# Performance work log

Measured on AMD Instinct MI355X. Metric: run time of the kernel, lower is better.

Reference implementation:

```python
import jax, jax.numpy as jnp
import numpy as np

SH_C0 = 0.28209479177387814
EPS2D = 0.3      # gsplat low-pass filter added to 2D covariance diagonal
NEAR = 0.01
ALPHA_MIN = 1.0 / 255.0
ALPHA_MAX = 0.999


def setup_inputs() -> dict:
    key = jax.random.key(0)
    ks = jax.random.split(key, 5)
    N = 2048
    means = 0.1 * jax.random.normal(ks[0], (N, 3), jnp.float32)
    quats = jax.random.normal(ks[1], (N, 4), jnp.float32)
    scales = -2.3 + 0.3 * jax.random.normal(ks[2], (N, 3), jnp.float32)
    opacities = -1.0 + 0.5 * jax.random.normal(ks[3], (N,), jnp.float32)
    sh_coeffs = jax.random.normal(ks[4], (N, 1, 3), jnp.float32)
    viewmats = jnp.eye(4, dtype=jnp.float32).at[2, 3].set(2.0)[None]  # [1,4,4] world->cam
    Ks = jnp.array([[[150.0, 0.0, 64.0], [0.0, 150.0, 64.0], [0.0, 0.0, 1.0]]], jnp.float32)
    return dict(means=means, quats=quats, scales=scales, opacities=opacities,
                sh_coeffs=sh_coeffs, viewmats=viewmats, Ks=Ks, width=128, height=128)


def _splat_render(means, quats, scales, opacities, sh_coeffs, viewmats, Ks, width, height):
    # --- parameter activations (GaussianSplat.activated_parameters) ---
    quats = quats / jnp.linalg.norm(quats, axis=-1, keepdims=True)
    scales = jnp.minimum(jnp.exp(scales), 10.0)
    opac = jax.nn.sigmoid(opacities)                                  # [N]
    colors = jnp.maximum(sh_coeffs[:, 0, :] * SH_C0 + 0.5, 0.0)       # [N,3] sh_degree=0

    # --- 3D covariance from quaternion (w,x,y,z) and scale ---
    w, x, y, z = quats[:, 0], quats[:, 1], quats[:, 2], quats[:, 3]
    R = jnp.stack([
        1 - 2 * (y * y + z * z), 2 * (x * y - w * z), 2 * (x * z + w * y),
        2 * (x * y + w * z), 1 - 2 * (x * x + z * z), 2 * (y * z - w * x),
        2 * (x * z - w * y), 2 * (y * z + w * x), 1 - 2 * (x * x + y * y)],
        axis=-1).reshape(-1, 3, 3)                                    # [N,3,3]
    M = R * scales[:, None, :]                                        # R @ diag(s)
    cov3d = jnp.einsum('nij,nkj->nik', M, M)                          # [N,3,3]

    # --- project to camera frame ---
    Rcw = viewmats[:, :3, :3]                                         # [C,3,3]
    tcw = viewmats[:, :3, 3]                                          # [C,3]
    p_cam = jnp.einsum('cij,nj->cni', Rcw, means) + tcw[:, None, :]   # [C,N,3]
    Vc = jnp.einsum('cij,njk,clk->cnil', Rcw, cov3d, Rcw)             # [C,N,3,3]

    xc, yc, zc = p_cam[..., 0], p_cam[..., 1], p_cam[..., 2]
    valid = zc > NEAR
    zs = jnp.where(valid, zc, 1.0)
    rz = 1.0 / zs
    fx = Ks[:, 0, 0][:, None]; fy = Ks[:, 1, 1][:, None]
    cx = Ks[:, 0, 2][:, None]; cy = Ks[:, 1, 2][:, None]
    u = fx * xc * rz + cx                                             # [C,N]
    v = fy * yc * rz + cy

    # --- EWA 2D covariance: J Vc J^T + eps2d*I, J = d(proj)/d(p_cam) ---
    J00 = fx * rz; J02 = -fx * xc * rz * rz
    J11 = fy * rz; J12 = -fy * yc * rz * rz
    V00, V01, V02 = Vc[..., 0, 0], Vc[..., 0, 1], Vc[..., 0, 2]
    V11, V12, V22 = Vc[..., 1, 1], Vc[..., 1, 2], Vc[..., 2, 2]
    a = J00 * J00 * V00 + 2 * J00 * J02 * V02 + J02 * J02 * V22 + EPS2D
    b = J00 * (J11 * V01 + J12 * V02) + J02 * (J11 * V12 + J12 * V22)
    c = J11 * J11 * V11 + 2 * J11 * J12 * V12 + J12 * J12 * V22 + EPS2D
    det = a * c - b * b
    valid = valid & (det > 0)
    det_s = jnp.where(valid, det, 1.0)
    conA = c / det_s; conB = -b / det_s; conC = a / det_s             # conic (inverse cov)

    # --- per-pixel gaussian evaluation (pixel centers at +0.5) ---
    px = jnp.arange(width, dtype=jnp.float32) + 0.5                   # [W]
    py = jnp.arange(height, dtype=jnp.float32) + 0.5                  # [H]
    dx = px[None, None, :] - u[..., None]                             # [C,N,W]
    dy = py[None, None, :] - v[..., None]                             # [C,N,H]
    sigma = (0.5 * (conA[..., None, None] * (dx * dx)[:, :, None, :]
                    + conC[..., None, None] * (dy * dy)[..., None])
             + conB[..., None, None] * dy[..., None] * dx[:, :, None, :])  # [C,N,H,W]
    alpha = opac[None, :, None, None] * jnp.exp(-sigma)
    alpha = jnp.minimum(alpha, ALPHA_MAX)
    alpha = jnp.where(valid[..., None, None] & (alpha >= ALPHA_MIN), alpha, 0.0)

    # --- front-to-back alpha compositing in depth order ---
    order = jnp.argsort(jnp.where(valid, zc, jnp.inf), axis=1)        # [C,N]
    alpha_s = jnp.take_along_axis(alpha, order[:, :, None, None], axis=1)
    colors_s = jnp.take_along_axis(jnp.broadcast_to(colors[None], (alpha.shape[0],) + colors.shape),
                                   order[:, :, None], axis=1)         # [C,N,3]
    logT = jnp.cumsum(jnp.log1p(-alpha_s), axis=1)
    logT_excl = jnp.pad(logT, ((0, 0), (1, 0), (0, 0), (0, 0)))[:, :-1]
    weights = alpha_s * jnp.exp(logT_excl)                            # [C,N,H,W]
    img = jnp.einsum('cnhw,cnk->chwk', weights, colors_s)             # [C,H,W,3]
    return img


def reference(means, quats, scales, opacities, sh_coeffs, viewmats, Ks, width, height):
    return _splat_render(means, quats, scales, opacities, sh_coeffs, viewmats, Ks, width, height)
```

## Files before the change

### kernel.cpp

```cpp
#include <hip/hip_runtime.h>
#include <math.h>

#define SH_C0     0.28209479177387814f
#define EPS2D     0.3f
#define NEARZ     0.01f
#define ALPHA_MIN (1.0f/255.0f)
#define ALPHA_MAX 0.999f
#define LOG2E     1.4426950408889634f

#define SEGS   32
#define HSEG   16

__global__ __launch_bounds__(256) void prep_rank_kernel(
        const float* __restrict__ means,
        const float* __restrict__ quats,
        const float* __restrict__ scales,
        const float* __restrict__ opacities,
        const float* __restrict__ sh,
        const float* __restrict__ vm,
        const float* __restrict__ K,
        float* __restrict__ sorted,
        int N) {
    int wave = blockIdx.x * 4 + (threadIdx.x >> 6);
    int lane = threadIdx.x & 63;
    if (wave >= N) return;
    int i = wave;

    float r00=vm[0], r01=vm[1], r02=vm[2],  t0=vm[3];
    float r10=vm[4], r11=vm[5], r12=vm[6],  t1=vm[7];
    float r20=vm[8], r21=vm[9], r22=vm[10], t2=vm[11];

    float mx = means[3*i+0], my = means[3*i+1], mz = means[3*i+2];
    float zci = r20*mx + r21*my + r22*mz + t2;
    float keyi = (zci > NEARZ) ? zci : INFINITY;
    int cnt = 0;
    for (int j = lane; j < N; j += 64) {
        float ax = means[3*j+0], ay = means[3*j+1], az = means[3*j+2];
        float zcj = r20*ax + r21*ay + r22*az + t2;
        float keyj = (zcj > NEARZ) ? zcj : INFINITY;
        cnt += (keyj < keyi) || (keyj == keyi && j < i);
    }
    #pragma unroll
    for (int off = 32; off > 0; off >>= 1)
        cnt += __shfl_xor(cnt, off, 64);

    float qw = quats[4*i+0], qx = quats[4*i+1], qy = quats[4*i+2], qz = quats[4*i+3];
    float rqn = rsqrtf(qw*qw + qx*qx + qy*qy + qz*qz);
    qw *= rqn; qx *= rqn; qy *= rqn; qz *= rqn;

    float R00 = 1.f - 2.f*(qy*qy + qz*qz);
    float R01 = 2.f*(qx*qy - qw*qz);
    float R02 = 2.f*(qx*qz + qw*qy);
    float R10 = 2.f*(qx*qy + qw*qz);
    float R11 = 1.f - 2.f*(qx*qx + qz*qz);
    float R12 = 2.f*(qy*qz - qw*qx);
    float R20 = 2.f*(qx*qz - qw*qy);
    float R21 = 2.f*(qy*qz + qw*qx);
    float R22 = 1.f - 2.f*(qx*qx + qy*qy);

    float s0 = fminf(expf(scales[3*i+0]), 10.f);
    float s1 = fminf(expf(scales[3*i+1]), 10.f);
    float s2 = fminf(expf(scales[3*i+2]), 10.f);

    float M00=R00*s0, M01=R01*s1, M02=R02*s2;
    float M10=R10*s0, M11=R11*s1, M12=R12*s2;
    float M20=R20*s0, M21=R21*s1, M22=R22*s2;

    float c00 = M00*M00 + M01*M01 + M02*M02;
    float c01 = M00*M10 + M01*M11 + M02*M12;
    float c02 = M00*M20 + M01*M21 + M02*M22;
    float c11 = M10*M10 + M11*M11 + M12*M12;
    float c12 = M10*M20 + M11*M21 + M12*M22;
    float c22 = M20*M20 + M21*M21 + M22*M22;

    float xc = r00*mx + r01*my + r02*mz + t0;
    float yc = r10*mx + r11*my + r12*mz + t1;
    float zc = zci;

    float T00 = r00*c00 + r01*c01 + r02*c02;
    float T01 = r00*c01 + r01*c11 + r02*c12;
    float T02 = r00*c02 + r01*c12 + r02*c22;
    float T10 = r10*c00 + r11*c01 + r12*c02;
    float T11 = r10*c01 + r11*c11 + r12*c12;
    float T12 = r10*c02 + r11*c12 + r12*c22;
    float T20 = r20*c00 + r21*c01 + r22*c02;
    float T21 = r20*c01 + r21*c11 + r22*c12;
    float T22 = r20*c02 + r21*c12 + r22*c22;
    float V00 = T00*r00 + T01*r01 + T02*r02;
    float V01 = T00*r10 + T01*r11 + T02*r12;
    float V02 = T00*r20 + T01*r21 + T02*r22;
    float V11 = T10*r10 + T11*r11 + T12*r12;
    float V12 = T10*r20 + T11*r21 + T12*r22;
    float V22 = T20*r20 + T21*r21 + T22*r22;

    float fx = K[0], cx = K[2], fy = K[4], cy = K[5];

    bool valid = zc > NEARZ;
    float zs = valid ? zc : 1.0f;
    float rz = 1.0f / zs;
    float u = fx*xc*rz + cx;
    float v = fy*yc*rz + cy;
    float J00 = fx*rz;
    float J02 = -fx*xc*rz*rz;
    float J11 = fy*rz;
    float J12 = -fy*yc*rz*rz;

    float a = J00*J00*V00 + 2.f*J00*J02*V02 + J02*J02*V22 + EPS2D;
    float b = J00*(J11*V01 + J12*V02) + J02*(J11*V12 + J12*V22);
    float c = J11*J11*V11 + 2.f*J11*J12*V12 + J12*J12*V22 + EPS2D;
    float det = a*c - b*b;
    valid = valid && (det > 0.f);
    float det_s = valid ? det : 1.0f;
    float conA =  c / det_s;
    float conB = -b / det_s;
    float conC =  a / det_s;

    float op  = 1.0f / (1.0f + expf(-opacities[i]));
    float cr = fmaxf(sh[3*i+0]*SH_C0 + 0.5f, 0.f);
    float cg = fmaxf(sh[3*i+1]*SH_C0 + 0.5f, 0.f);
    float cb = fmaxf(sh[3*i+2]*SH_C0 + 0.5f, 0.f);

    float e0, e1, e2, e3, e4, e5;
    if (valid) {
        e0 = u; e1 = v;
        e2 = 0.5f*conA*LOG2E; e3 = conB*LOG2E; e4 = 0.5f*conC*LOG2E;
        e5 = log2f(op);
    } else {
        e0=0; e1=0; e2=0; e3=0; e4=0; e5=-1.0e4f;
    }

    if (lane < 16) {
        float val;
        switch (lane) {
            case 0: val = e0; break;
            case 1: val = e1; break;
            case 2: val = e2; break;
            case 3: val = e3; break;
            case 4: val = e4; break;
            case 5: val = e5; break;
            case 6: val = cr; break;
            case 7: val = cg; break;
            case 8: val = cb; break;
            default: val = 0.f; break;
        }
        sorted[16*(size_t)cnt + lane] = val;
    }
}

__global__ __launch_bounds__(1024) void render_main_kernel(
        const float* __restrict__ sorted,
        float4* __restrict__ parts,
        int N, int P) {
    __shared__ float4 part[HSEG][64];
    int tid  = threadIdx.x;
    int lane = tid & 63;
    int w    = __builtin_amdgcn_readfirstlane(tid >> 6);
    int h    = blockIdx.x & 1;
    int pg   = blockIdx.x >> 1;
    int p    = pg * 64 + lane;

    int y = p >> 7;
    int x = p & 127;
    float px = (float)x + 0.5f;
    float py = (float)y + 0.5f;

    int chunk = (N + SEGS - 1) / SEGS;
    int s  = h * HSEG + w;
    int g0 = s * chunk;
    int g1 = min(g0 + chunk, N);

    float accr = 0.f, accg = 0.f, accb = 0.f, T = 1.f;
    #pragma unroll 4
    for (int g = g0; g < g1; ++g) {
        const float* d = sorted + 16*(size_t)g;
        float u  = d[0], v  = d[1];
        float A2 = d[2], B  = d[3], C2 = d[4], lop = d[5];
        float cr = d[6], cg = d[7], cb = d[8];
        float dx = px - u, dy = py - v;
        float t2  = fmaf(A2, dx, B*dy);
        float arg = fmaf(-C2, dy*dy, lop);
        arg = fmaf(-dx, t2, arg);
        float al = exp2f(arg);
        al = fminf(al, ALPHA_MAX);
        al = (al >= ALPHA_MIN) ? al : 0.f;
        float wgt = T * al;
        accr = fmaf(wgt, cr, accr);
        accg = fmaf(wgt, cg, accg);
        accb = fmaf(wgt, cb, accb);
        T = fmaf(-al, T, T);
    }
    part[w][lane] = make_float4(accr, accg, accb, T);
    __syncthreads();

    if (tid < 64) {
        float R = 0.f, G = 0.f, Bc = 0.f, Tr = 1.f;
        #pragma unroll
        for (int ss = 0; ss < HSEG; ++ss) {
            float4 q = part[ss][tid];
            R  = fmaf(Tr, q.x, R);
            G  = fmaf(Tr, q.y, G);
            Bc = fmaf(Tr, q.z, Bc);
            Tr *= q.w;
        }
        parts[(size_t)h * P + p] = make_float4(R, G, Bc, Tr);
    }
}

__global__ __launch_bounds__(256) void combine_kernel(
        const float4* __restrict__ parts,
        float* __restrict__ out, int P) {
    int p = blockIdx.x * 256 + threadIdx.x;
    if (p >= P) return;
    float4 a = parts[p];
    float4 b = parts[(size_t)P + p];
    out[3*(size_t)p+0] = fmaf(a.w, b.x, a.x);
    out[3*(size_t)p+1] = fmaf(a.w, b.y, a.y);
    out[3*(size_t)p+2] = fmaf(a.w, b.z, a.z);
}

extern "C" void kernel_launch(void* const* d_in, const int* in_sizes, int n_in,
                              void* d_out, int out_size, void* d_ws, size_t ws_size,
                              hipStream_t stream) {
    const float* means     = (const float*)d_in[0];
    const float* quats     = (const float*)d_in[1];
    const float* scales    = (const float*)d_in[2];
    const float* opacities = (const float*)d_in[3];
    const float* sh        = (const float*)d_in[4];
    const float* vm        = (const float*)d_in[5];
    const float* K         = (const float*)d_in[6];

    int N = in_sizes[0] / 3;
    int P = out_size / 3;

    float*  sorted = (float*)d_ws;
    float4* parts  = (float4*)((float*)d_ws + (size_t)N * 16);

    prep_rank_kernel<<<(N + 3) / 4, 256, 0, stream>>>(
        means, quats, scales, opacities, sh, vm, K, sorted, N);
    render_main_kernel<<<((P + 63) / 64) * 2, 1024, 0, stream>>>(
        sorted, parts, N, P);
    combine_kernel<<<(P + 255) / 256, 256, 0, stream>>>(
        parts, (float*)d_out, P);
}
```

Measured before the change: 102.8 us.

## Split render into four 512-thread layers with packed 48-byte float4 records

The render kernel moves from two 1024-thread halves to four 512-thread layers of 8 waves each, and the combine kernel now composites four partial layers. Gaussian records shrink from 16 to 12 floats and are read as three float4 loads. Opacity is stored linearly and multiplied after a raw hardware exp2, so the per-gaussian add of log-opacity becomes a multiply. The aim is better occupancy and fewer load instructions, at the cost of more combine traffic and slightly different alpha rounding.

Measured after the change: 95.46 us. -7.2%, faster.

```diff
diff --git a/kernel.cpp b/kernel.cpp
--- a/kernel.cpp
+++ b/kernel.cpp
@@ -9,7 +9,8 @@
 #define LOG2E     1.4426950408889634f
 
 #define SEGS   32
-#define HSEG   16
+#define LSEG   8
+#define NLAYER 4
 
 __global__ __launch_bounds__(256) void prep_rank_kernel(
         const float* __restrict__ means,
@@ -124,69 +125,69 @@
     if (valid) {
         e0 = u; e1 = v;
         e2 = 0.5f*conA*LOG2E; e3 = conB*LOG2E; e4 = 0.5f*conC*LOG2E;
-        e5 = log2f(op);
+        e5 = op;
     } else {
-        e0=0; e1=0; e2=0; e3=0; e4=0; e5=-1.0e4f;
-    }
-
-    if (lane < 16) {
+        e0=0; e1=0; e2=0; e3=0; e4=0; e5=0;
+    }
+
+    if (lane < 12) {
         float val;
         switch (lane) {
-            case 0: val = e0; break;
-            case 1: val = e1; break;
-            case 2: val = e2; break;
-            case 3: val = e3; break;
-            case 4: val = e4; break;
-            case 5: val = e5; break;
-            case 6: val = cr; break;
-            case 7: val = cg; break;
-            case 8: val = cb; break;
+            case 0:  val = e0; break;
+            case 1:  val = e1; break;
+            case 2:  val = e2; break;
+            case 3:  val = e3; break;
+            case 4:  val = e4; break;
+            case 5:  val = e5; break;
+            case 6:  val = cr; break;
+            case 7:  val = cg; break;
+            case 8:  val = cb; break;
             default: val = 0.f; break;
         }
-        sorted[16*(size_t)cnt + lane] = val;
-    }
-}
-
-__global__ __launch_bounds__(1024) void render_main_kernel(
+        sorted[12*(size_t)cnt + lane] = val;
+    }
+}
+
+__global__ __launch_bounds__(512, 8) void render_main_kernel(
         const float* __restrict__ sorted,
         float4* __restrict__ parts,
         int N, int P) {
-    __shared__ float4 part[HSEG][64];
+    __shared__ float4 part[LSEG][64];
     int tid  = threadIdx.x;
     int lane = tid & 63;
     int w    = __builtin_amdgcn_readfirstlane(tid >> 6);
-    int h    = blockIdx.x & 1;
-    int pg   = blockIdx.x >> 1;
+    int L    = blockIdx.x & (NLAYER - 1);
+    int pg   = blockIdx.x >> 2;
     int p    = pg * 64 + lane;
 
-    int y = p >> 7;
-    int x = p & 127;
-    float px = (float)x + 0.5f;
-    float py = (float)y + 0.5f;
+    float px = (float)(p & 127) + 0.5f;
+    float py = (float)(p >> 7) + 0.5f;
 
     int chunk = (N + SEGS - 1) / SEGS;
-    int s  = h * HSEG + w;
+    int s  = L * LSEG + w;
     int g0 = s * chunk;
     int g1 = min(g0 + chunk, N);
 
+    const float4* rec = (const float4*)sorted + 3*(size_t)g0;
+
     float accr = 0.f, accg = 0.f, accb = 0.f, T = 1.f;
-    #pragma unroll 4
+    #pragma unroll 2
     for (int g = g0; g < g1; ++g) {
-        const float* d = sorted + 16*(size_t)g;
-        float u  = d[0], v  = d[1];
-        float A2 = d[2], B  = d[3], C2 = d[4], lop = d[5];
-        float cr = d[6], cg = d[7], cb = d[8];
-        float dx = px - u, dy = py - v;
-        float t2  = fmaf(A2, dx, B*dy);
-        float arg = fmaf(-C2, dy*dy, lop);
-        arg = fmaf(-dx, t2, arg);
-        float al = exp2f(arg);
+        float4 r0 = rec[0];
+        float4 r1 = rec[1];
+        float  cb = rec[2].x;
+        rec += 3;
+        float dx = px - r0.x, dy = py - r0.y;
+        float t2 = fmaf(r0.z, dx, r0.w * dy);
+        float m  = dx * t2;
+        float arg = fmaf(-r1.x, dy*dy, -m);
+        float al = r1.y * __builtin_amdgcn_exp2f(arg);
         al = fminf(al, ALPHA_MAX);
         al = (al >= ALPHA_MIN) ? al : 0.f;
         float wgt = T * al;
-        accr = fmaf(wgt, cr, accr);
-        accg = fmaf(wgt, cg, accg);
-        accb = fmaf(wgt, cb, accb);
+        accr = fmaf(wgt, r1.z, accr);
+        accg = fmaf(wgt, r1.w, accg);
+        accb = fmaf(wgt, cb,  accb);
         T = fmaf(-al, T, T);
     }
     part[w][lane] = make_float4(accr, accg, accb, T);
@@ -195,14 +196,14 @@
     if (tid < 64) {
         float R = 0.f, G = 0.f, Bc = 0.f, Tr = 1.f;
         #pragma unroll
-        for (int ss = 0; ss < HSEG; ++ss) {
+        for (int ss = 0; ss < LSEG; ++ss) {
             float4 q = part[ss][tid];
             R  = fmaf(Tr, q.x, R);
             G  = fmaf(Tr, q.y, G);
             Bc = fmaf(Tr, q.z, Bc);
             Tr *= q.w;
         }
-        parts[(size_t)h * P + p] = make_float4(R, G, Bc, Tr);
+        parts[(size_t)L * P + p] = make_float4(R, G, Bc, Tr);
     }
 }
 
@@ -211,11 +212,18 @@
         float* __restrict__ out, int P) {
     int p = blockIdx.x * 256 + threadIdx.x;
     if (p >= P) return;
-    float4 a = parts[p];
-    float4 b = parts[(size_t)P + p];
-    out[3*(size_t)p+0] = fmaf(a.w, b.x, a.x);
-    out[3*(size_t)p+1] = fmaf(a.w, b.y, a.y);
-    out[3*(size_t)p+2] = fmaf(a.w, b.z, a.z);
+    float R = 0.f, G = 0.f, B = 0.f, Tr = 1.f;
+    #pragma unroll
+    for (int l = 0; l < NLAYER; ++l) {
+        float4 q = parts[(size_t)l * P + p];
+        R  = fmaf(Tr, q.x, R);
+        G  = fmaf(Tr, q.y, G);
+        B  = fmaf(Tr, q.z, B);
+        Tr *= q.w;
+    }
+    out[3*(size_t)p+0] = R;
+    out[3*(size_t)p+1] = G;
+    out[3*(size_t)p+2] = B;
 }
 
 extern "C" void kernel_launch(void* const* d_in, const int* in_sizes, int n_in,
@@ -233,11 +241,11 @@
     int P = out_size / 3;
 
     float*  sorted = (float*)d_ws;
-    float4* parts  = (float4*)((float*)d_ws + (size_t)N * 16);
+    float4* parts  = (float4*)((float*)d_ws + (size_t)N * 12);
 
     prep_rank_kernel<<<(N + 3) / 4, 256, 0, stream>>>(
         means, quats, scales, opacities, sh, vm, K, sorted, N);
-    render_main_kernel<<<((P + 63) / 64) * 2, 1024, 0, stream>>>(
+    render_main_kernel<<<((P + 63) / 64) * NLAYER, 512, 0, stream>>>(
         sorted, parts, N, P);
     combine_kernel<<<(P + 255) / 256, 256, 0, stream>>>(
         parts, (float*)d_out, P);
```
